# Performance work log

Hardware: AMD Instinct MI355X
Metric: run time of the kernel (lower is better)

The kernel has to match this reference:

```python
import jax, jax.numpy as jnp
import numpy as np

N_NODES = 50000
N_EDGES = 800000
N_GRAPHS = 512


def gcn_conv(x, W, b, src, dst, n_nodes):
    # Standard PyG GCNConv: linear transform, add self-loops, D^-1/2 (A+I) D^-1/2 aggregation.
    x = x @ W  # [N, out]
    loop = jnp.arange(n_nodes, dtype=src.dtype)
    s = jnp.concatenate([src, loop])  # [E+N]
    d = jnp.concatenate([dst, loop])
    deg = jax.ops.segment_sum(jnp.ones_like(d, dtype=x.dtype), d, num_segments=n_nodes)
    dinv = jnp.where(deg > 0, jax.lax.rsqrt(jnp.maximum(deg, 1e-12)), 0.0)
    norm = dinv[s] * dinv[d]  # [E+N]
    msg = x[s] * norm[:, None]  # gather + scale
    out = jax.ops.segment_sum(msg, d, num_segments=n_nodes)  # scatter-add
    return out + b


def setup_inputs() -> dict:
    key = jax.random.key(0)
    ks = jax.random.split(key, 10)
    x = jax.random.normal(ks[0], (N_NODES, 128), dtype=jnp.float32)
    edge_index = jax.random.randint(ks[1], (2, N_EDGES), 0, N_NODES, dtype=jnp.int64)
    batch = jnp.sort(jax.random.randint(ks[2], (N_NODES,), 0, N_GRAPHS, dtype=jnp.int64))
    y = jax.random.randint(ks[3], (N_GRAPHS,), 0, 4, dtype=jnp.int64)
    W1 = jax.random.normal(ks[4], (128, 64), dtype=jnp.float32) * (1.0 / np.sqrt(128))
    b1 = jnp.zeros((64,), dtype=jnp.float32)
    W2 = jax.random.normal(ks[5], (64, 64), dtype=jnp.float32) * (1.0 / np.sqrt(64))
    b2 = jnp.zeros((64,), dtype=jnp.float32)
    Wfc = jax.random.normal(ks[6], (64, 4), dtype=jnp.float32) * (1.0 / np.sqrt(64))
    bfc = jnp.zeros((4,), dtype=jnp.float32)
    return {"x": x, "edge_index": edge_index, "batch": batch, "y": y,
            "W1": W1, "b1": b1, "W2": W2, "b2": b2, "Wfc": Wfc, "bfc": bfc}


def reference(x, edge_index, batch, y, W1, b1, W2, b2, Wfc, bfc):
    src, dst = edge_index[0], edge_index[1]
    h = jax.nn.relu(gcn_conv(x, W1, b1, src, dst, N_NODES))
    h = jax.nn.relu(gcn_conv(h, W2, b2, src, dst, N_NODES))
    # global mean pool over graph ids
    sums = jax.ops.segment_sum(h, batch, num_segments=N_GRAPHS)  # [G, out]
    cnts = jax.ops.segment_sum(jnp.ones((h.shape[0],), h.dtype), batch, num_segments=N_GRAPHS)
    pooled = sums / jnp.maximum(cnts, 1.0)[:, None]
    logits = pooled @ Wfc + bfc
    logp = jax.nn.log_softmax(logits, axis=1)
    return (logp, y)
```

## Files before the change

### kernel.cpp

```cpp
#include <hip/hip_runtime.h>
#include <hip/hip_fp16.h>
#include <math.h>

#define N_NODES 50000
#define N_EDGES 800000
#define N_GRAPHS 512
#define NBKT 196
#define SENT N_NODES
#define EPB 2048
#define NSEG 391
#define CAP_C 48
#define NBLK_B2 392
#define CAP_SH 8192
#define NBLK_GM 782
#define PREP_GRID (NBLK_B2 + NBLK_GM)
#define N_GROUPS 6272
#define NBLK_G 1568

typedef float v2f __attribute__((ext_vector_type(2)));
typedef float f32x4 __attribute__((ext_vector_type(4)));
typedef short s16x8 __attribute__((ext_vector_type(8)));

#define OFF_DINV    0u
#define OFF_GGRP    200704u
#define OFF_CNTM    250880u
#define OFF_TMP     557568u
#define OFF_SORTED  15271680u
#define OFF_XS8_1   28116736u
#define OFF_XS8_2   31316992u
#define OFF_H2      34517248u

__device__ __forceinline__ unsigned short f2bf(float f) {
    unsigned int u = __float_as_uint(f);
    u += 0x7FFFu + ((u >> 16) & 1u);
    return (unsigned short)(u >> 16);
}

__global__ __launch_bounds__(256) void binA(const int* __restrict__ src, const int* __restrict__ dst,
                                            int* __restrict__ cntmat, unsigned int* __restrict__ tmp,
                                            unsigned int* __restrict__ x1, unsigned int* __restrict__ x2,
                                            float* __restrict__ dinv) {
    __shared__ int cnt[256];
    int t = threadIdx.x;
    cnt[t] = 0;
    if (blockIdx.x == 0) {
        if (t < 16) x1[N_NODES * 16 + t] = 0;
        else if (t < 32) x2[N_NODES * 16 + (t - 16)] = 0;
        else if (t == 32) dinv[SENT] = 0.0f;
    }
    __syncthreads();
    int e0 = blockIdx.x * EPB;
#pragma unroll
    for (int i = 0; i < 8; ++i) {
        int e = e0 + i * 256 + t;
        if (e < N_EDGES) {
            int s = src[e], d = dst[e];
            int b = d >> 8;
            int p = atomicAdd(&cnt[b], 1);
            tmp[(b * NSEG + blockIdx.x) * CAP_C + p] =
                (unsigned int)s | ((unsigned int)(d & 255) << 17);
        }
    }
    __syncthreads();
    if (t < NBKT) cntmat[blockIdx.x * NBKT + t] = cnt[t];
}

__global__ __launch_bounds__(256) void prep(const unsigned int* __restrict__ tmp,
                                            const int* __restrict__ cntmat,
                                            int* __restrict__ sorted, int2* __restrict__ ggrp,
                                            float* __restrict__ dinv,
                                            const float* __restrict__ X, const float* __restrict__ W1,
                                            unsigned int* __restrict__ xs8) {
    __shared__ __align__(16) char pool[34816];
    __shared__ int bad;
    int t = threadIdx.x;

    if (blockIdx.x < NBLK_B2) {
        int* cnt  = (int*)pool;
        int* lbs  = (int*)(pool + 512);
        int* cur  = (int*)(pool + 1024);
        int* gK   = (int*)(pool + 1536);
        int* gpre = (int*)(pool + 1600);
        int* ldsS = (int*)(pool + 1792);
        int b2 = blockIdx.x, bkt = b2 >> 1, half = b2 & 1;
        if (t < 128) cnt[t] = 0;
        __syncthreads();
        for (int seg = t; seg < NSEG; seg += 256) {
            int c = cntmat[seg * NBKT + bkt];
            const unsigned int* tp = tmp + (bkt * NSEG + seg) * CAP_C;
            for (int e = 0; e < c; ++e) {
                int d = (int)(tp[e] >> 17);
                if ((d >> 7) == half) atomicAdd(&cnt[d & 127], 1);
            }
        }
        __syncthreads();
        int node = 0, deg = 0, K = 0, KP = 0, lb = 0, myreal = 0;
        if (t < 128) {
            node = bkt * 256 + half * 128 + t;
            myreal = node < N_NODES;
            deg = cnt[t];
            int count = myreal ? deg + 1 : 0;
            int mx = count;
            mx = max(mx, __shfl_xor(mx, 1));
            mx = max(mx, __shfl_xor(mx, 2));
            mx = max(mx, __shfl_xor(mx, 4));
            K = (mx + 3) & ~3;
            KP = K + 4;
            if ((t & 7) == 0) gK[t >> 3] = KP;
        }
        __syncthreads();
        if (t == 0) {
            int s = 0;
#pragma unroll
            for (int g = 0; g < 16; ++g) { gpre[g] = s; s += gK[g]; }
            gpre[16] = s;
        }
        __syncthreads();
        if (t < 128) {
            lb = 8 * gpre[t >> 3] + (t & 7);
            lbs[t] = lb;
            cur[t] = myreal ? 1 : 0;
            if (myreal) {
                dinv[node] = rsqrtf(1.0f + (float)deg);
                ldsS[lb] = node;
            }
            if ((t & 7) == 0)
                ggrp[b2 * 16 + (t >> 3)] = make_int2(b2 * CAP_SH + 8 * gpre[t >> 3], K);
        }
        __syncthreads();
        for (int seg = t; seg < NSEG; seg += 256) {
            int c = cntmat[seg * NBKT + bkt];
            const unsigned int* tp = tmp + (bkt * NSEG + seg) * CAP_C;
            for (int e = 0; e < c; ++e) {
                unsigned int pk = tp[e];
                int d = (int)(pk >> 17);
                if ((d >> 7) == half) {
                    int loc = d & 127;
                    int j = atomicAdd(&cur[loc], 1);
                    ldsS[lbs[loc] + j * 8] = (int)(pk & 0x1FFFFu);
                }
            }
        }
        __syncthreads();
        if (t < 128)
            for (int j = cur[t]; j < KP; ++j) ldsS[lb + j * 8] = SENT;
        __syncthreads();
        int ptot = 8 * gpre[16];
        int4* dst4 = (int4*)(sorted + b2 * CAP_SH);
        const int4* src4 = (const int4*)ldsS;
        for (int p = t; p < (ptot >> 2); p += 256) dst4[p] = src4[p];
    } else {
        short* W1T = (short*)pool;
        float* sD  = (float*)(pool + 17408);
        int gb = blockIdx.x - NBLK_B2;
        int row0 = gb * 64;
        for (int i = t; i < 8192; i += 256) {
            int k = i >> 6, c = i & 63;
            W1T[c * 136 + k] = (short)f2bf(W1[i]);
        }
        __syncthreads();
        int w = t >> 6, lane = t & 63;
        int arow = lane & 15, kg = lane >> 4;
        int r = row0 + w * 16 + arow;
        const float* xp = X + r * 128 + kg * 8;
        bool vr = (r < N_NODES);
        const short* wb = &W1T[arow * 136 + kg * 8];
        f32x4 ac0 = {0.f, 0.f, 0.f, 0.f}, ac1 = ac0, ac2 = ac0, ac3 = ac0;
#pragma unroll
        for (int kk = 0; kk < 4; ++kk) {
            float4 xa, xb;
            if (vr) { xa = *(const float4*)(xp); xb = *(const float4*)(xp + 4); }
            else    { xa = make_float4(0.f, 0.f, 0.f, 0.f); xb = xa; }
            xp += 32;
            s16x8 af;
            af[0] = (short)f2bf(xa.x); af[1] = (short)f2bf(xa.y);
            af[2] = (short)f2bf(xa.z); af[3] = (short)f2bf(xa.w);
            af[4] = (short)f2bf(xb.x); af[5] = (short)f2bf(xb.y);
            af[6] = (short)f2bf(xb.z); af[7] = (short)f2bf(xb.w);
            const short* wk = wb + kk * 32;
            s16x8 bf0 = *(const s16x8*)(wk);
            s16x8 bf1 = *(const s16x8*)(wk + 16 * 136);
            s16x8 bf2 = *(const s16x8*)(wk + 32 * 136);
            s16x8 bf3 = *(const s16x8*)(wk + 48 * 136);
            asm volatile(
                "s_nop 1\n\t"
                "v_mfma_f32_16x16x32_bf16 %0, %4, %5, %0\n\t"
                "v_mfma_f32_16x16x32_bf16 %1, %4, %6, %1\n\t"
                "v_mfma_f32_16x16x32_bf16 %2, %4, %7, %2\n\t"
                "v_mfma_f32_16x16x32_bf16 %3, %4, %8, %3"
                : "+v"(ac0), "+v"(ac1), "+v"(ac2), "+v"(ac3)
                : "v"(af), "v"(bf0), "v"(bf1), "v"(bf2), "v"(bf3));
        }
        asm volatile("s_nop 7\n\ts_nop 7");
        int dr = w * 16 + kg * 4;
#pragma unroll
        for (int reg = 0; reg < 4; ++reg) {
            sD[(dr + reg) * 68 + arow]      = ac0[reg];
            sD[(dr + reg) * 68 + 16 + arow] = ac1[reg];
            sD[(dr + reg) * 68 + 32 + arow] = ac2[reg];
            sD[(dr + reg) * 68 + 48 + arow] = ac3[reg];
        }
        __syncthreads();
        if (t == 0) {
            float r0v = 0.f, r1v = 0.f;
            const float* x0 = X + row0 * 128;
            for (int k = 0; k < 128; ++k) {
                float wv = W1[k * 64];
                r0v += x0[k] * wv;
                r1v += x0[128 + k] * wv;
            }
            bad = (fabsf(r0v - sD[0])  > 0.05f * fabsf(r0v) + 0.1f) ||
                  (fabsf(r1v - sD[68]) > 0.05f * fabsf(r1v) + 0.1f);
        }
        __syncthreads();
        if (bad) {
            for (int i = t; i < 4096; i += 256) {
                int lr = i >> 6, c = i & 63;
                int nd = row0 + lr;
                if (nd < N_NODES) {
                    const float* xr2 = X + nd * 128;
                    float s = 0.f;
                    for (int k = 0; k < 128; ++k) s += xr2[k] * W1[k * 64 + c];
                    sD[lr * 68 + c] = s;
                }
            }
            __syncthreads();
        }
        for (int i = t; i < 1024; i += 256) {
            int lr = i >> 4, q = i & 15;
            int nd = row0 + lr;
            if (nd < N_NODES) {
                float4 v = *(const float4*)&sD[lr * 68 + q * 4];
                unsigned int pk = 0;
                pk = __builtin_amdgcn_cvt_pk_fp8_f32(v.x, v.y, pk, false);
                pk = __builtin_amdgcn_cvt_pk_fp8_f32(v.z, v.w, pk, true);
                xs8[nd * 16 + q] = pk;
            }
        }
    }
}

#define FMA_ROW(rv, ds) { \
    v2f f0 = __builtin_amdgcn_cvt_pk_f32_fp8((rv).x, false); \
    v2f f1 = __builtin_amdgcn_cvt_pk_f32_fp8((rv).x, true); \
    v2f f2 = __builtin_amdgcn_cvt_pk_f32_fp8((rv).y, false); \
    v2f f3 = __builtin_amdgcn_cvt_pk_f32_fp8((rv).y, true); \
    a0 += f0.x * (ds); a1 += f0.y * (ds); a2 += f1.x * (ds); a3 += f1.y * (ds); \
    a4 += f2.x * (ds); a5 += f2.y * (ds); a6 += f3.x * (ds); a7 += f3.y * (ds); }

#define GATHER_ACC() \
    int lane = threadIdx.x & 63; \
    int sub = lane >> 3, frag = lane & 7; \
    int node = grp * 8 + sub; \
    int2 gi = ggrp[grp]; \
    int K = gi.y; \
    const int* sp = sorted + gi.x + sub; \
    const uint2* xr = (const uint2*)xs8 + frag; \
    float a0 = 0, a1 = 0, a2 = 0, a3 = 0, a4 = 0, a5 = 0, a6 = 0, a7 = 0; \
    int i0 = sp[0], i1 = sp[8], i2 = sp[16], i3 = sp[24]; \
    for (int k = 0; k < K; k += 4) { \
        uint2 r0 = xr[i0 * 8]; \
        uint2 r1 = xr[i1 * 8]; \
        uint2 r2 = xr[i2 * 8]; \
        uint2 r3 = xr[i3 * 8]; \
        float s0 = dinv[i0], s1 = dinv[i1], s2 = dinv[i2], s3 = dinv[i3]; \
        const int* np = sp + (k + 4) * 8; \
        i0 = np[0]; i1 = np[8]; i2 = np[16]; i3 = np[24]; \
        FMA_ROW(r0, s0); FMA_ROW(r1, s1); FMA_ROW(r2, s2); FMA_ROW(r3, s3); \
    }

__global__ __launch_bounds__(256) void gather_fuse(const unsigned char* __restrict__ xs8,
                                                   const int2* __restrict__ ggrp,
                                                   const int* __restrict__ sorted,
                                                   const float* __restrict__ dinv,
                                                   const float* __restrict__ bias,
                                                   const float* __restrict__ W2,
                                                   unsigned int* __restrict__ xs8o) {
    __shared__ float sW2[64 * 64];
    __shared__ float sH[32][68];
    {
        const float4* ws = (const float4*)W2;
        float4* wd = (float4*)sW2;
        for (int i = threadIdx.x; i < 1024; i += 256) wd[i] = ws[i];
    }
    int wvl = threadIdx.x >> 6;
    int grp = blockIdx.x * 4 + wvl;

    GATHER_ACC()

    {
        float dv = dinv[node];
        float4 bA = *(const float4*)(bias + frag * 8);
        float4 bB = *(const float4*)(bias + frag * 8 + 4);
        float4 w0, w1;
        w0.x = fmaxf(a0 * dv + bA.x, 0.0f); w0.y = fmaxf(a1 * dv + bA.y, 0.0f);
        w0.z = fmaxf(a2 * dv + bA.z, 0.0f); w0.w = fmaxf(a3 * dv + bA.w, 0.0f);
        w1.x = fmaxf(a4 * dv + bB.x, 0.0f); w1.y = fmaxf(a5 * dv + bB.y, 0.0f);
        w1.z = fmaxf(a6 * dv + bB.z, 0.0f); w1.w = fmaxf(a7 * dv + bB.w, 0.0f);
        *(float4*)&sH[wvl * 8 + sub][frag * 8] = w0;
        *(float4*)&sH[wvl * 8 + sub][frag * 8 + 4] = w1;
    }
    __syncthreads();
    int r = threadIdx.x >> 3;
    int cg = (threadIdx.x & 7) * 8;
    float b0 = 0, b1 = 0, b2 = 0, b3 = 0, b4 = 0, b5 = 0, b6 = 0, b7 = 0;
#pragma unroll 8
    for (int k = 0; k < 64; ++k) {
        float hv = sH[r][k];
        float4 wa = *(const float4*)&sW2[k * 64 + cg];
        float4 wbv = *(const float4*)&sW2[k * 64 + cg + 4];
        b0 += hv * wa.x; b1 += hv * wa.y; b2 += hv * wa.z; b3 += hv * wa.w;
        b4 += hv * wbv.x; b5 += hv * wbv.y; b6 += hv * wbv.z; b7 += hv * wbv.w;
    }
    int node2 = blockIdx.x * 32 + r;
    if (node2 < N_NODES) {
        unsigned int p0 = 0, p1 = 0;
        p0 = __builtin_amdgcn_cvt_pk_fp8_f32(b0, b1, p0, false);
        p0 = __builtin_amdgcn_cvt_pk_fp8_f32(b2, b3, p0, true);
        p1 = __builtin_amdgcn_cvt_pk_fp8_f32(b4, b5, p1, false);
        p1 = __builtin_amdgcn_cvt_pk_fp8_f32(b6, b7, p1, true);
        *(uint2*)(xs8o + node2 * 16 + (cg >> 2)) = make_uint2(p0, p1);
    }
}

__global__ __launch_bounds__(256) void gather_h2(const unsigned char* __restrict__ xs8,
                                                 const int2* __restrict__ ggrp,
                                                 const int* __restrict__ sorted,
                                                 const float* __restrict__ dinv,
                                                 const float* __restrict__ bias,
                                                 __half* __restrict__ h2) {
    int grp = blockIdx.x * 4 + (threadIdx.x >> 6);

    GATHER_ACC()

    if (node < N_NODES) {
        float dv = dinv[node];
        float4 bA = *(const float4*)(bias + frag * 8);
        float4 bB = *(const float4*)(bias + frag * 8 + 4);
        float v0 = fmaxf(a0 * dv + bA.x, 0.0f), v1 = fmaxf(a1 * dv + bA.y, 0.0f);
        float v2 = fmaxf(a2 * dv + bA.z, 0.0f), v3 = fmaxf(a3 * dv + bA.w, 0.0f);
        float v4 = fmaxf(a4 * dv + bB.x, 0.0f), v5 = fmaxf(a5 * dv + bB.y, 0.0f);
        float v6 = fmaxf(a6 * dv + bB.z, 0.0f), v7 = fmaxf(a7 * dv + bB.w, 0.0f);
        __half2 p0 = __floats2half2_rn(v0, v1), p1 = __floats2half2_rn(v2, v3);
        __half2 p2 = __floats2half2_rn(v4, v5), p3 = __floats2half2_rn(v6, v7);
        uint4 pk;
        pk.x = *(unsigned int*)&p0; pk.y = *(unsigned int*)&p1;
        pk.z = *(unsigned int*)&p2; pk.w = *(unsigned int*)&p3;
        *(uint4*)(h2 + node * 64 + frag * 8) = pk;
    }
}

__device__ __forceinline__ int lower_bound(const int* __restrict__ a, int n, int v) {
    int lo = 0, hi = n;
    while (lo < hi) { int m = (lo + hi) >> 1; if (a[m] < v) lo = m + 1; else hi = m; }
    return lo;
}

__global__ __launch_bounds__(256) void pool_head(const __half* __restrict__ h2,
                                                 const int* __restrict__ batch,
                                                 const float* __restrict__ Wfc, const float* __restrict__ bfc,
                                                 const int* __restrict__ y, float* __restrict__ out) {
    __shared__ int s_beg, s_end;
    __shared__ float sh[4][64];
    __shared__ float pl[64];
    __shared__ float lg[4];
    int g = blockIdx.x;
    int t = threadIdx.x;
    if (t == 0) s_beg = lower_bound(batch, N_NODES, g);
    if (t == 1) s_end = lower_bound(batch, N_NODES, g + 1);
    __syncthreads();
    int beg = s_beg, end = s_end;
    int f = t & 63, seg = t >> 6;
    float s = 0.0f;
    for (int r = beg + seg; r < end; r += 4) s += __half2float(h2[r * 64 + f]);
    sh[seg][f] = s;
    __syncthreads();
    if (t < 64) {
        float p = sh[0][t] + sh[1][t] + sh[2][t] + sh[3][t];
        pl[t] = p / fmaxf((float)(end - beg), 1.0f);
    }
    __syncthreads();
    if (t < 4) {
        float l = bfc[t];
#pragma unroll
        for (int k = 0; k < 64; ++k) l += pl[k] * Wfc[k * 4 + t];
        lg[t] = l;
    }
    __syncthreads();
    if (t == 0) {
        float l0 = lg[0], l1 = lg[1], l2 = lg[2], l3 = lg[3];
        float m = fmaxf(fmaxf(l0, l1), fmaxf(l2, l3));
        float ss = expf(l0 - m) + expf(l1 - m) + expf(l2 - m) + expf(l3 - m);
        float lse = m + logf(ss);
        out[g * 4 + 0] = l0 - lse;
        out[g * 4 + 1] = l1 - lse;
        out[g * 4 + 2] = l2 - lse;
        out[g * 4 + 3] = l3 - lse;
        out[N_GRAPHS * 4 + g] = (float)y[g];
    }
}

extern "C" void kernel_launch(void* const* d_in, const int* in_sizes, int n_in,
                              void* d_out, int out_size, void* d_ws, size_t ws_size,
                              hipStream_t stream) {
    const float* x     = (const float*)d_in[0];
    const int*   ei    = (const int*)d_in[1];
    const int*   batch = (const int*)d_in[2];
    const int*   y     = (const int*)d_in[3];
    const float* W1    = (const float*)d_in[4];
    const float* b1    = (const float*)d_in[5];
    const float* W2    = (const float*)d_in[6];
    const float* b2    = (const float*)d_in[7];
    const float* Wfc   = (const float*)d_in[8];
    const float* bfc   = (const float*)d_in[9];
    float* out = (float*)d_out;

    const int* src = ei;
    const int* dst = ei + N_EDGES;

    char* wsb = (char*)d_ws;
    float*        dinv   = (float*)(wsb + OFF_DINV);
    int2*         ggrp   = (int2*)(wsb + OFF_GGRP);
    int*          cntmat = (int*)(wsb + OFF_CNTM);
    unsigned int* tmp    = (unsigned int*)(wsb + OFF_TMP);
    int*          sorted = (int*)(wsb + OFF_SORTED);
    unsigned int* xs8_1  = (unsigned int*)(wsb + OFF_XS8_1);
    unsigned int* xs8_2  = (unsigned int*)(wsb + OFF_XS8_2);
    __half*       h2     = (__half*)(wsb + OFF_H2);

    binA<<<NSEG, 256, 0, stream>>>(src, dst, cntmat, tmp, xs8_1, xs8_2, dinv);
    prep<<<PREP_GRID, 256, 0, stream>>>(tmp, cntmat, sorted, ggrp, dinv, x, W1, xs8_1);
    gather_fuse<<<NBLK_G, 256, 0, stream>>>((const unsigned char*)xs8_1, ggrp, sorted,
                                            dinv, b1, W2, xs8_2);
    gather_h2<<<NBLK_G, 256, 0, stream>>>((const unsigned char*)xs8_2, ggrp, sorted,
                                          dinv, b2, h2);
    pool_head<<<N_GRAPHS, 256, 0, stream>>>(h2, batch, Wfc, bfc, y, out);
}
```

Baseline: 173.0 us.

## Fuse layer-2 gather with mean pooling and head via atomics and last-block finish

```diff
diff --git a/kernel.cpp b/kernel.cpp
--- a/kernel.cpp
+++ b/kernel.cpp
@@ -15,6 +15,7 @@
 #define NBLK_GM 782
 #define PREP_GRID (NBLK_B2 + NBLK_GM)
 #define N_GROUPS 6272
+#define N_GROUPS_REAL 6250
 #define NBLK_G 1568
 
 typedef float v2f __attribute__((ext_vector_type(2)));
@@ -28,7 +29,8 @@
 #define OFF_SORTED  15271680u
 #define OFF_XS8_1   28116736u
 #define OFF_XS8_2   31316992u
-#define OFF_H2      34517248u
+#define OFF_POOL    34517248u
+#define OFF_CTR     34648320u
 
 __device__ __forceinline__ unsigned short f2bf(float f) {
     unsigned int u = __float_as_uint(f);
@@ -39,14 +41,17 @@
 __global__ __launch_bounds__(256) void binA(const int* __restrict__ src, const int* __restrict__ dst,
                                             int* __restrict__ cntmat, unsigned int* __restrict__ tmp,
                                             unsigned int* __restrict__ x1, unsigned int* __restrict__ x2,
-                                            float* __restrict__ dinv) {
+                                            float* __restrict__ dinv, float* __restrict__ pooled,
+                                            int* __restrict__ ctr) {
     __shared__ int cnt[256];
     int t = threadIdx.x;
     cnt[t] = 0;
+    if (blockIdx.x < 128) pooled[blockIdx.x * 256 + t] = 0.0f;
     if (blockIdx.x == 0) {
         if (t < 16) x1[N_NODES * 16 + t] = 0;
         else if (t < 32) x2[N_NODES * 16 + (t - 16)] = 0;
         else if (t == 32) dinv[SENT] = 0.0f;
+        else if (t == 33) *ctr = 0;
     }
     __syncthreads();
     int e0 = blockIdx.x * EPB;
@@ -72,7 +77,6 @@
                                             const float* __restrict__ X, const float* __restrict__ W1,
                                             unsigned int* __restrict__ xs8) {
     __shared__ __align__(16) char pool[34816];
-    __shared__ int bad;
     int t = threadIdx.x;
 
     if (blockIdx.x < NBLK_B2) {
@@ -201,31 +205,6 @@
             sD[(dr + reg) * 68 + 48 + arow] = ac3[reg];
         }
         __syncthreads();
-        if (t == 0) {
-            float r0v = 0.f, r1v = 0.f;
-            const float* x0 = X + row0 * 128;
-            for (int k = 0; k < 128; ++k) {
-                float wv = W1[k * 64];
-                r0v += x0[k] * wv;
-                r1v += x0[128 + k] * wv;
-            }
-            bad = (fabsf(r0v - sD[0])  > 0.05f * fabsf(r0v) + 0.1f) ||
-                  (fabsf(r1v - sD[68]) > 0.05f * fabsf(r1v) + 0.1f);
-        }
-        __syncthreads();
-        if (bad) {
-            for (int i = t; i < 4096; i += 256) {
-                int lr = i >> 6, c = i & 63;
-                int nd = row0 + lr;
-                if (nd < N_NODES) {
-                    const float* xr2 = X + nd * 128;
-                    float s = 0.f;
-                    for (int k = 0; k < 128; ++k) s += xr2[k] * W1[k * 64 + c];
-                    sD[lr * 68 + c] = s;
-                }
-            }
-            __syncthreads();
-        }
         for (int i = t; i < 1024; i += 256) {
             int lr = i >> 4, q = i & 15;
             int nd = row0 + lr;
@@ -240,6 +219,14 @@
     }
 }
 
+#define ADD_ROW(rv) { \
+    v2f f0 = __builtin_amdgcn_cvt_pk_f32_fp8((rv).x, false); \
+    v2f f1 = __builtin_amdgcn_cvt_pk_f32_fp8((rv).x, true); \
+    v2f f2 = __builtin_amdgcn_cvt_pk_f32_fp8((rv).y, false); \
+    v2f f3 = __builtin_amdgcn_cvt_pk_f32_fp8((rv).y, true); \
+    a0 += f0.x; a1 += f0.y; a2 += f1.x; a3 += f1.y; \
+    a4 += f2.x; a5 += f2.y; a6 += f3.x; a7 += f3.y; }
+
 #define FMA_ROW(rv, ds) { \
     v2f f0 = __builtin_amdgcn_cvt_pk_f32_fp8((rv).x, false); \
     v2f f1 = __builtin_amdgcn_cvt_pk_f32_fp8((rv).x, true); \
@@ -247,27 +234,6 @@
     v2f f3 = __builtin_amdgcn_cvt_pk_f32_fp8((rv).y, true); \
     a0 += f0.x * (ds); a1 += f0.y * (ds); a2 += f1.x * (ds); a3 += f1.y * (ds); \
     a4 += f2.x * (ds); a5 += f2.y * (ds); a6 += f3.x * (ds); a7 += f3.y * (ds); }
-
-#define GATHER_ACC() \
-    int lane = threadIdx.x & 63; \
-    int sub = lane >> 3, frag = lane & 7; \
-    int node = grp * 8 + sub; \
-    int2 gi = ggrp[grp]; \
-    int K = gi.y; \
-    const int* sp = sorted + gi.x + sub; \
-    const uint2* xr = (const uint2*)xs8 + frag; \
-    float a0 = 0, a1 = 0, a2 = 0, a3 = 0, a4 = 0, a5 = 0, a6 = 0, a7 = 0; \
-    int i0 = sp[0], i1 = sp[8], i2 = sp[16], i3 = sp[24]; \
-    for (int k = 0; k < K; k += 4) { \
-        uint2 r0 = xr[i0 * 8]; \
-        uint2 r1 = xr[i1 * 8]; \
-        uint2 r2 = xr[i2 * 8]; \
-        uint2 r3 = xr[i3 * 8]; \
-        float s0 = dinv[i0], s1 = dinv[i1], s2 = dinv[i2], s3 = dinv[i3]; \
-        const int* np = sp + (k + 4) * 8; \
-        i0 = np[0]; i1 = np[8]; i2 = np[16]; i3 = np[24]; \
-        FMA_ROW(r0, s0); FMA_ROW(r1, s1); FMA_ROW(r2, s2); FMA_ROW(r3, s3); \
-    }
 
 __global__ __launch_bounds__(256) void gather_fuse(const unsigned char* __restrict__ xs8,
                                                    const int2* __restrict__ ggrp,
@@ -286,7 +252,25 @@
     int wvl = threadIdx.x >> 6;
     int grp = blockIdx.x * 4 + wvl;
 
-    GATHER_ACC()
+    int lane = threadIdx.x & 63;
+    int sub = lane >> 3, frag = lane & 7;
+    int node = grp * 8 + sub;
+    int2 gi = ggrp[grp];
+    int K = gi.y;
+    const int* sp = sorted + gi.x + sub;
+    const uint2* xr = (const uint2*)xs8 + frag;
+    float a0 = 0, a1 = 0, a2 = 0, a3 = 0, a4 = 0, a5 = 0, a6 = 0, a7 = 0;
+    int i0 = sp[0], i1 = sp[8], i2 = sp[16], i3 = sp[24];
+    for (int k = 0; k < K; k += 4) {
+        uint2 r0 = xr[i0 * 8];
+        uint2 r1 = xr[i1 * 8];
+        uint2 r2 = xr[i2 * 8];
+        uint2 r3 = xr[i3 * 8];
+        float s0 = dinv[i0], s1 = dinv[i1], s2 = dinv[i2], s3 = dinv[i3];
+        const int* np = sp + (k + 4) * 8;
+        i0 = np[0]; i1 = np[8]; i2 = np[16]; i3 = np[24];
+        FMA_ROW(r0, s0); FMA_ROW(r1, s1); FMA_ROW(r2, s2); FMA_ROW(r3, s3);
+    }
 
     {
         float dv = dinv[node];
@@ -314,26 +298,55 @@
     }
     int node2 = blockIdx.x * 32 + r;
     if (node2 < N_NODES) {
+        float s = dinv[node2];
         unsigned int p0 = 0, p1 = 0;
-        p0 = __builtin_amdgcn_cvt_pk_fp8_f32(b0, b1, p0, false);
-        p0 = __builtin_amdgcn_cvt_pk_fp8_f32(b2, b3, p0, true);
-        p1 = __builtin_amdgcn_cvt_pk_fp8_f32(b4, b5, p1, false);
-        p1 = __builtin_amdgcn_cvt_pk_fp8_f32(b6, b7, p1, true);
+        p0 = __builtin_amdgcn_cvt_pk_fp8_f32(b0 * s, b1 * s, p0, false);
+        p0 = __builtin_amdgcn_cvt_pk_fp8_f32(b2 * s, b3 * s, p0, true);
+        p1 = __builtin_amdgcn_cvt_pk_fp8_f32(b4 * s, b5 * s, p1, false);
+        p1 = __builtin_amdgcn_cvt_pk_fp8_f32(b6 * s, b7 * s, p1, true);
         *(uint2*)(xs8o + node2 * 16 + (cg >> 2)) = make_uint2(p0, p1);
     }
 }
 
-__global__ __launch_bounds__(256) void gather_h2(const unsigned char* __restrict__ xs8,
-                                                 const int2* __restrict__ ggrp,
-                                                 const int* __restrict__ sorted,
-                                                 const float* __restrict__ dinv,
-                                                 const float* __restrict__ bias,
-                                                 __half* __restrict__ h2) {
+__device__ __forceinline__ int lower_bound(const int* __restrict__ a, int n, int v) {
+    int lo = 0, hi = n;
+    while (lo < hi) { int m = (lo + hi) >> 1; if (a[m] < v) lo = m + 1; else hi = m; }
+    return lo;
+}
+
+__global__ __launch_bounds__(256) void gather_pool(const unsigned char* __restrict__ xs8,
+                                                   const int2* __restrict__ ggrp,
+                                                   const int* __restrict__ sorted,
+                                                   const float* __restrict__ dinv,
+                                                   const float* __restrict__ bias,
+                                                   const int* __restrict__ batch,
+                                                   const float* __restrict__ Wfc,
+                                                   const float* __restrict__ bfc,
+                                                   const int* __restrict__ y,
+                                                   float* __restrict__ pooled,
+                                                   int* __restrict__ ctr,
+                                                   float* __restrict__ out) {
+    __shared__ int s_last;
     int grp = blockIdx.x * 4 + (threadIdx.x >> 6);
-
-    GATHER_ACC()
-
-    if (node < N_NODES) {
+    int lane = threadIdx.x & 63;
+    int sub = lane >> 3, frag = lane & 7;
+    int node = grp * 8 + sub;
+    int2 gi = ggrp[grp];
+    int K = gi.y;
+    const int* sp = sorted + gi.x + sub;
+    const uint2* xr = (const uint2*)xs8 + frag;
+    float a0 = 0, a1 = 0, a2 = 0, a3 = 0, a4 = 0, a5 = 0, a6 = 0, a7 = 0;
+    int i0 = sp[0], i1 = sp[8], i2 = sp[16], i3 = sp[24];
+    for (int k = 0; k < K; k += 4) {
+        uint2 r0 = xr[i0 * 8];
+        uint2 r1 = xr[i1 * 8];
+        uint2 r2 = xr[i2 * 8];
+        uint2 r3 = xr[i3 * 8];
+        const int* np = sp + (k + 4) * 8;
+        i0 = np[0]; i1 = np[8]; i2 = np[16]; i3 = np[24];
+        ADD_ROW(r0); ADD_ROW(r1); ADD_ROW(r2); ADD_ROW(r3);
+    }
+    if (grp < N_GROUPS_REAL) {
         float dv = dinv[node];
         float4 bA = *(const float4*)(bias + frag * 8);
         float4 bB = *(const float4*)(bias + frag * 8 + 4);
@@ -341,54 +354,43 @@
         float v2 = fmaxf(a2 * dv + bA.z, 0.0f), v3 = fmaxf(a3 * dv + bA.w, 0.0f);
         float v4 = fmaxf(a4 * dv + bB.x, 0.0f), v5 = fmaxf(a5 * dv + bB.y, 0.0f);
         float v6 = fmaxf(a6 * dv + bB.z, 0.0f), v7 = fmaxf(a7 * dv + bB.w, 0.0f);
-        __half2 p0 = __floats2half2_rn(v0, v1), p1 = __floats2half2_rn(v2, v3);
-        __half2 p2 = __floats2half2_rn(v4, v5), p3 = __floats2half2_rn(v6, v7);
-        uint4 pk;
-        pk.x = *(unsigned int*)&p0; pk.y = *(unsigned int*)&p1;
-        pk.z = *(unsigned int*)&p2; pk.w = *(unsigned int*)&p3;
-        *(uint4*)(h2 + node * 64 + frag * 8) = pk;
-    }
-}
-
-__device__ __forceinline__ int lower_bound(const int* __restrict__ a, int n, int v) {
-    int lo = 0, hi = n;
-    while (lo < hi) { int m = (lo + hi) >> 1; if (a[m] < v) lo = m + 1; else hi = m; }
-    return lo;
-}
-
-__global__ __launch_bounds__(256) void pool_head(const __half* __restrict__ h2,
-                                                 const int* __restrict__ batch,
-                                                 const float* __restrict__ Wfc, const float* __restrict__ bfc,
-                                                 const int* __restrict__ y, float* __restrict__ out) {
-    __shared__ int s_beg, s_end;
-    __shared__ float sh[4][64];
-    __shared__ float pl[64];
-    __shared__ float lg[4];
-    int g = blockIdx.x;
+        int g = batch[node];
+        if (__shfl(g, 0) == __shfl(g, 63)) {
+            v0 += __shfl_xor(v0, 8);  v1 += __shfl_xor(v1, 8);  v2 += __shfl_xor(v2, 8);  v3 += __shfl_xor(v3, 8);
+            v4 += __shfl_xor(v4, 8);  v5 += __shfl_xor(v5, 8);  v6 += __shfl_xor(v6, 8);  v7 += __shfl_xor(v7, 8);
+            v0 += __shfl_xor(v0, 16); v1 += __shfl_xor(v1, 16); v2 += __shfl_xor(v2, 16); v3 += __shfl_xor(v3, 16);
+            v4 += __shfl_xor(v4, 16); v5 += __shfl_xor(v5, 16); v6 += __shfl_xor(v6, 16); v7 += __shfl_xor(v7, 16);
+            v0 += __shfl_xor(v0, 32); v1 += __shfl_xor(v1, 32); v2 += __shfl_xor(v2, 32); v3 += __shfl_xor(v3, 32);
+            v4 += __shfl_xor(v4, 32); v5 += __shfl_xor(v5, 32); v6 += __shfl_xor(v6, 32); v7 += __shfl_xor(v7, 32);
+            if (sub == 0) {
+                float* pg = pooled + g * 64 + frag * 8;
+                atomicAdd(pg + 0, v0); atomicAdd(pg + 1, v1); atomicAdd(pg + 2, v2); atomicAdd(pg + 3, v3);
+                atomicAdd(pg + 4, v4); atomicAdd(pg + 5, v5); atomicAdd(pg + 6, v6); atomicAdd(pg + 7, v7);
+            }
+        } else {
+            float* pg = pooled + g * 64 + frag * 8;
+            atomicAdd(pg + 0, v0); atomicAdd(pg + 1, v1); atomicAdd(pg + 2, v2); atomicAdd(pg + 3, v3);
+            atomicAdd(pg + 4, v4); atomicAdd(pg + 5, v5); atomicAdd(pg + 6, v6); atomicAdd(pg + 7, v7);
+        }
+    }
+    __threadfence();
+    __syncthreads();
+    if (threadIdx.x == 0)
+        s_last = (atomicAdd(ctr, 1) == (int)gridDim.x - 1);
+    __syncthreads();
+    if (!s_last) return;
     int t = threadIdx.x;
-    if (t == 0) s_beg = lower_bound(batch, N_NODES, g);
-    if (t == 1) s_end = lower_bound(batch, N_NODES, g + 1);
-    __syncthreads();
-    int beg = s_beg, end = s_end;
-    int f = t & 63, seg = t >> 6;
-    float s = 0.0f;
-    for (int r = beg + seg; r < end; r += 4) s += __half2float(h2[r * 64 + f]);
-    sh[seg][f] = s;
-    __syncthreads();
-    if (t < 64) {
-        float p = sh[0][t] + sh[1][t] + sh[2][t] + sh[3][t];
-        pl[t] = p / fmaxf((float)(end - beg), 1.0f);
-    }
-    __syncthreads();
-    if (t < 4) {
-        float l = bfc[t];
-#pragma unroll
-        for (int k = 0; k < 64; ++k) l += pl[k] * Wfc[k * 4 + t];
-        lg[t] = l;
-    }
-    __syncthreads();
-    if (t == 0) {
-        float l0 = lg[0], l1 = lg[1], l2 = lg[2], l3 = lg[3];
+    for (int g = t; g < N_GRAPHS; g += 256) {
+        int beg = lower_bound(batch, N_NODES, g);
+        int end = lower_bound(batch, N_NODES, g + 1);
+        float inv = 1.0f / fmaxf((float)(end - beg), 1.0f);
+        float l0 = bfc[0], l1 = bfc[1], l2 = bfc[2], l3 = bfc[3];
+#pragma unroll 8
+        for (int k = 0; k < 64; ++k) {
+            float p = atomicAdd(&pooled[g * 64 + k], 0.0f) * inv;
+            l0 += p * Wfc[k * 4 + 0]; l1 += p * Wfc[k * 4 + 1];
+            l2 += p * Wfc[k * 4 + 2]; l3 += p * Wfc[k * 4 + 3];
+        }
         float m = fmaxf(fmaxf(l0, l1), fmaxf(l2, l3));
         float ss = expf(l0 - m) + expf(l1 - m) + expf(l2 - m) + expf(l3 - m);
         float lse = m + logf(ss);
@@ -426,13 +428,13 @@
     int*          sorted = (int*)(wsb + OFF_SORTED);
     unsigned int* xs8_1  = (unsigned int*)(wsb + OFF_XS8_1);
     unsigned int* xs8_2  = (unsigned int*)(wsb + OFF_XS8_2);
-    __half*       h2     = (__half*)(wsb + OFF_H2);
-
-    binA<<<NSEG, 256, 0, stream>>>(src, dst, cntmat, tmp, xs8_1, xs8_2, dinv);
+    float*        pooled = (float*)(wsb + OFF_POOL);
+    int*          ctr    = (int*)(wsb + OFF_CTR);
+
+    binA<<<NSEG, 256, 0, stream>>>(src, dst, cntmat, tmp, xs8_1, xs8_2, dinv, pooled, ctr);
     prep<<<PREP_GRID, 256, 0, stream>>>(tmp, cntmat, sorted, ggrp, dinv, x, W1, xs8_1);
     gather_fuse<<<NBLK_G, 256, 0, stream>>>((const unsigned char*)xs8_1, ggrp, sorted,
                                             dinv, b1, W2, xs8_2);
-    gather_h2<<<NBLK_G, 256, 0, stream>>>((const unsigned char*)xs8_2, ggrp, sorted,
-                                          dinv, b2, h2);
-    pool_head<<<N_GRAPHS, 256, 0, stream>>>(h2, batch, Wfc, bfc, y, out);
-}
+    gather_pool<<<NBLK_G, 256, 0, stream>>>((const unsigned char*)xs8_2, ggrp, sorted,
+                                            dinv, b2, batch, Wfc, bfc, y, pooled, ctr, out);
+}
```

New measurement: 332.3 us. +92.1%, slower.
